# Kernel optimization log

Hardware: AMD Instinct MI355X
Metric: run time of the kernel (lower is better)

Reference implementation:

```python
import jax, jax.numpy as jnp
import numpy as np

N, F_IN, H, O = 4096, 512, 4, 256
ALPHA = 0.2  # leaky-relu negative slope
NEG = -9e15  # mask value for non-edges (matches DAEGC)


def setup_inputs() -> dict:
    key = jax.random.key(0)
    ks = jax.random.split(key, 9)
    x = jax.random.normal(ks[0], (N, F_IN), jnp.float32)
    adj = (jax.random.uniform(ks[1], (N, N)) < 0.01).astype(jnp.float32)
    adj = jnp.maximum(adj, jnp.eye(N, dtype=jnp.float32))
    M = jax.random.uniform(ks[2], (N, N), dtype=jnp.float32)  # proximity matrix
    s0 = 1.0 / np.sqrt(F_IN)
    s1 = 1.0 / np.sqrt(H * O)
    W0 = jax.random.normal(ks[3], (H, F_IN, O), jnp.float32) * s0
    a_self0 = jax.random.normal(ks[4], (H, O), jnp.float32) * 0.1
    a_neigh0 = jax.random.normal(ks[5], (H, O), jnp.float32) * 0.1
    W1 = jax.random.normal(ks[6], (H, H * O, O), jnp.float32) * s1
    a_self1 = jax.random.normal(ks[7], (H, O), jnp.float32) * 0.1
    a_neigh1 = jax.random.normal(ks[8], (H, O), jnp.float32) * 0.1
    return dict(x=x, adj=adj, M=M, W0=W0, a_self0=a_self0, a_neigh0=a_neigh0,
                W1=W1, a_self1=a_self1, a_neigh1=a_neigh1)


def gat_layer(x, adj, M, W, a_s, a_n, concat):
    # x: [N, F_in], W: [H, F_in, O]
    h = jnp.einsum('nf,hfo->hno', x, W)                      # [H, N, O]
    e = (jnp.einsum('hno,ho->hn', h, a_s)[:, :, None]
         + jnp.einsum('hno,ho->hn', h, a_n)[:, None, :])     # [H, N, N]
    e = jax.nn.leaky_relu(e * M[None], ALPHA)
    e = jnp.where(adj[None] > 0, e, NEG)
    attn = jax.nn.softmax(e, axis=-1)                        # masked neighbor softmax
    out = jnp.einsum('hnm,hmo->hno', attn, h)                # [H, N, O]
    if concat:
        return jax.nn.elu(out.transpose(1, 0, 2).reshape(x.shape[0], -1))  # [N, H*O]
    return out.mean(axis=0)                                  # [N, O]


def reference(x, adj, M, W0, a_self0, a_neigh0, W1, a_self1, a_neigh1):
    h = gat_layer(x, adj, M, W0, a_self0, a_neigh0, True)
    h = gat_layer(h, adj, M, W1, a_self1, a_neigh1, False)
    # F.normalize(h, p=2, dim=1) with eps=1e-12
    z = h / jnp.maximum(jnp.linalg.norm(h, axis=1, keepdims=True), 1e-12)
    A_pred = jax.nn.sigmoid(z @ z.T)                          # dot-product decode [N, N]
    return (A_pred, z)
```

## Files before the change

### kernel.cpp

```cpp
#include <hip/hip_runtime.h>
#include <hip/hip_bf16.h>
#include <math.h>

#define N_NODES 4096
#define F_IN0   512
#define HEADS   4
#define O_DIM   256
#define HO      1024
#define LRELU_A 0.2f
#define MAXE    192
#define LOG2E   1.44269504088896f

typedef __bf16 bf16_t;
typedef bf16_t bf16x8 __attribute__((ext_vector_type(8)));
typedef float f32x4 __attribute__((ext_vector_type(4)));
typedef unsigned short u16x8 __attribute__((ext_vector_type(8)));

__device__ __forceinline__ unsigned short f2b(float f) {
    __hip_bfloat16 t = __float2bfloat16(f);
    return __builtin_bit_cast(unsigned short, t);
}
__device__ __forceinline__ float b2f(unsigned short u) {
    unsigned int v = ((unsigned int)u) << 16;
    return __builtin_bit_cast(float, v);
}
__device__ __forceinline__ float fexp(float x) {
    return __builtin_amdgcn_exp2f(x * LOG2E);
}
__device__ __forceinline__ float fsigmoid(float x) {
    return __builtin_amdgcn_rcpf(1.f + __builtin_amdgcn_exp2f(-x * LOG2E));
}

#define GLOAD_LDS(g, l) \
    __builtin_amdgcn_global_load_lds((const __attribute__((address_space(1))) unsigned int*)(g), \
                                     (__attribute__((address_space(3))) unsigned int*)(l), 16, 0, 0)

__device__ __forceinline__ void transpose_tile(const float* __restrict__ W,
                                               unsigned short* __restrict__ Wt,
                                               int K, int O, int kt, int ot, int h,
                                               float (*t)[33], int tid) {
    const float* Wh = W + (size_t)h * K * O;
    unsigned short* Wth = Wt + (size_t)h * K * O;
    const int k0 = kt * 32, o0 = ot * 32;
    const int tx = tid & 31, ty = tid >> 5;
    for (int r = ty; r < 32; r += 8) t[r][tx] = Wh[(size_t)(k0 + r) * O + o0 + tx];
    __syncthreads();
    for (int r = ty; r < 32; r += 8)
        Wth[(size_t)(o0 + r) * K + k0 + tx] = f2b(t[tx][r]);
}

__global__ __launch_bounds__(256) void conv_k(const float* __restrict__ x,
                                              const float* __restrict__ W0,
                                              const float* __restrict__ W1,
                                              unsigned short* __restrict__ xb,
                                              unsigned short* __restrict__ wt0,
                                              unsigned short* __restrict__ wt1) {
    __shared__ float t[32][33];
    const int b = blockIdx.x;
    const int tid = threadIdx.x;
    if (b < 2048) {
        int i = b * 256 + tid;
        float4 v = ((const float4*)x)[i];
        ushort4 o;
        o.x = f2b(v.x); o.y = f2b(v.y); o.z = f2b(v.z); o.w = f2b(v.w);
        ((ushort4*)xb)[i] = o;
    } else if (b < 2560) {
        int b2 = b - 2048;
        transpose_tile(W0, wt0, F_IN0, O_DIM, (b2 & 15), ((b2 >> 4) & 7), b2 >> 7, t, tid);
    } else {
        int b2 = b - 2560;
        transpose_tile(W1, wt1, HO, O_DIM, (b2 & 31), ((b2 >> 5) & 7), b2 >> 8, t, tid);
    }
}

__global__ __launch_bounds__(256) void edge_k(const float* __restrict__ adj,
                                              int* __restrict__ ecnt,
                                              int* __restrict__ eidx) {
    const int w    = threadIdx.x >> 6;
    const int lane = threadIdx.x & 63;
    const int n    = blockIdx.x * 4 + w;
    const float* adjr = adj + (size_t)n * N_NODES;
    float4 a4[16];
#pragma unroll
    for (int it = 0; it < 16; ++it)
        a4[it] = *(const float4*)&adjr[lane * 4 + it * 256];
    unsigned long long mask = 0;
#pragma unroll
    for (int it = 0; it < 16; ++it) {
        if (a4[it].x > 0.f) mask |= 1ull << (it * 4 + 0);
        if (a4[it].y > 0.f) mask |= 1ull << (it * 4 + 1);
        if (a4[it].z > 0.f) mask |= 1ull << (it * 4 + 2);
        if (a4[it].w > 0.f) mask |= 1ull << (it * 4 + 3);
    }
    const int ec = __popcll(mask);
    int sc = ec;
#pragma unroll
    for (int off = 1; off < 64; off <<= 1) {
        int u = __shfl_up(sc, off, 64);
        if (lane >= off) sc += u;
    }
    int base = sc - ec;
    unsigned long long mm = mask;
    while (mm) {
        const int q = __builtin_ctzll(mm);
        mm &= mm - 1;
        const int m = lane * 4 + ((q >> 2) << 8) + (q & 3);
        eidx[(size_t)n * MAXE + base] = m;
        ++base;
    }
    if (lane == 63) ecnt[n] = sc;
}

__global__ __launch_bounds__(256) void mfma_nt(const bf16_t* __restrict__ A,
                                               const bf16_t* __restrict__ B,
                                               unsigned short* __restrict__ Cv,
                                               int K, int ldc,
                                               unsigned long long bStride,
                                               unsigned long long cStride) {
    B += blockIdx.z * bStride;
    const size_t zoff = (size_t)blockIdx.z * cStride;
    __shared__ bf16_t sA[128 * 32];
    __shared__ bf16_t sB[128 * 32];
    const int tid  = threadIdx.x;
    const int lane = tid & 63;
    const int wave = tid >> 6;
    const int wr = (wave >> 1) * 64;
    const int wc = (wave & 1) * 64;
    const int rowBase = blockIdx.x * 128;
    const int colBase = blockIdx.y * 128;
    const int l15  = lane & 15;
    const int quad = lane >> 4;

    const int sm = tid & 127;
    const int sc = tid >> 7;
    const bf16_t* aRow = A + (size_t)(rowBase + sm) * K + sc * 8;
    const bf16_t* bRow = B + (size_t)(colBase + sm) * K + sc * 8;
    bf16_t* sA0 = &sA[(tid & ~63) * 8];
    bf16_t* sA1 = &sA[(256 + (tid & ~63)) * 8];
    bf16_t* sB0 = &sB[(tid & ~63) * 8];
    bf16_t* sB1 = &sB[(256 + (tid & ~63)) * 8];

    f32x4 acc[4][4] = {};

    for (int k0 = 0; k0 < K; k0 += 32) {
        GLOAD_LDS(aRow + k0,      sA0);
        GLOAD_LDS(aRow + k0 + 16, sA1);
        GLOAD_LDS(bRow + k0,      sB0);
        GLOAD_LDS(bRow + k0 + 16, sB1);
        __syncthreads();
        bf16x8 af[4], bfr[4];
#pragma unroll
        for (int i = 0; i < 4; ++i) {
            af[i]  = *(bf16x8*)&sA[(quad * 128 + wr + i * 16 + l15) * 8];
            bfr[i] = *(bf16x8*)&sB[(quad * 128 + wc + i * 16 + l15) * 8];
        }
#pragma unroll
        for (int i = 0; i < 4; ++i)
#pragma unroll
            for (int j = 0; j < 4; ++j)
                acc[i][j] = __builtin_amdgcn_mfma_f32_16x16x32_bf16(af[i], bfr[j], acc[i][j], 0, 0, 0);
        __syncthreads();
    }

    const int orow = rowBase + wr + quad * 4;
    const int ocol = colBase + wc + l15;
#pragma unroll
    for (int i = 0; i < 4; ++i)
#pragma unroll
        for (int j = 0; j < 4; ++j)
#pragma unroll
            for (int r = 0; r < 4; ++r)
                Cv[zoff + (size_t)(orow + i * 16 + r) * ldc + ocol + j * 16] = f2b(acc[i][j][r]);
}

#define EP_STRIDE 132
__global__ __launch_bounds__(256) void decode_k(const bf16_t* __restrict__ Z,
                                                float* __restrict__ out) {
    __shared__ float smem_f[32 * EP_STRIDE];
    bf16_t* sA = (bf16_t*)smem_f;
    bf16_t* sB = (bf16_t*)(smem_f + 2048);
    float*  sE = smem_f;

    const int tid  = threadIdx.x;
    const int lane = tid & 63;
    const int wave = tid >> 6;
    const int wr = (wave >> 1) * 64;
    const int wc = (wave & 1) * 64;
    const int rowBase = blockIdx.x * 128;
    const int colBase = blockIdx.y * 128;
    const int l15  = lane & 15;
    const int quad = lane >> 4;

    const int sm = tid & 127;
    const int sc = tid >> 7;
    const bf16_t* aRow = Z + (size_t)(rowBase + sm) * O_DIM + sc * 8;
    const bf16_t* bRow = Z + (size_t)(colBase + sm) * O_DIM + sc * 8;
    bf16_t* sA0 = &sA[(tid & ~63) * 8];
    bf16_t* sA1 = &sA[(256 + (tid & ~63)) * 8];
    bf16_t* sB0 = &sB[(tid & ~63) * 8];
    bf16_t* sB1 = &sB[(256 + (tid & ~63)) * 8];

    f32x4 acc[4][4] = {};

    for (int k0 = 0; k0 < O_DIM; k0 += 32) {
        GLOAD_LDS(aRow + k0,      sA0);
        GLOAD_LDS(aRow + k0 + 16, sA1);
        GLOAD_LDS(bRow + k0,      sB0);
        GLOAD_LDS(bRow + k0 + 16, sB1);
        __syncthreads();
        bf16x8 af[4], bfr[4];
#pragma unroll
        for (int i = 0; i < 4; ++i) {
            af[i]  = *(bf16x8*)&sA[(quad * 128 + wr + i * 16 + l15) * 8];
            bfr[i] = *(bf16x8*)&sB[(quad * 128 + wc + i * 16 + l15) * 8];
        }
#pragma unroll
        for (int i = 0; i < 4; ++i)
#pragma unroll
            for (int j = 0; j < 4; ++j)
                acc[i][j] = __builtin_amdgcn_mfma_f32_16x16x32_bf16(af[i], bfr[j], acc[i][j], 0, 0, 0);
        __syncthreads();
    }

    const int lrBase = (wave >> 1) * 16;
    for (int i = 0; i < 4; ++i) {
#pragma unroll
        for (int j = 0; j < 4; ++j)
#pragma unroll
            for (int r = 0; r < 4; ++r)
                sE[(lrBase + quad * 4 + r) * EP_STRIDE + wc + j * 16 + l15] = acc[i][j][r];
        __syncthreads();
#pragma unroll
        for (int p = 0; p < 4; ++p) {
            const int idx4 = p * 256 + tid;
            const int lr = idx4 >> 5;
            const int c4 = idx4 & 31;
            f32x4 v = *(f32x4*)&sE[lr * EP_STRIDE + c4 * 4];
            f32x4 o;
            o[0] = fsigmoid(v[0]); o[1] = fsigmoid(v[1]);
            o[2] = fsigmoid(v[2]); o[3] = fsigmoid(v[3]);
            const int grow = rowBase + (lr >> 4) * 64 + i * 16 + (lr & 15);
            *(f32x4*)&out[(size_t)grow * N_NODES + colBase + c4 * 4] = o;
        }
        __syncthreads();
    }
}

__global__ __launch_bounds__(256) void scores_k(const unsigned short* __restrict__ hb,
                                                const float* __restrict__ a_s,
                                                const float* __restrict__ a_n,
                                                float* __restrict__ s_self4,
                                                float* __restrict__ s_neigh4) {
    const int n = blockIdx.x;
    const int head = threadIdx.x >> 6;
    const int lane = threadIdx.x & 63;
    const ushort4 hv = *(const ushort4*)&hb[(size_t)n * HO + head * O_DIM + lane * 4];
    const float4 av = *(const float4*)&a_s[head * O_DIM + lane * 4];
    const float4 nv = *(const float4*)&a_n[head * O_DIM + lane * 4];
    float h0 = b2f(hv.x), h1 = b2f(hv.y), h2 = b2f(hv.z), h3 = b2f(hv.w);
    float ps = h0 * av.x + h1 * av.y + h2 * av.z + h3 * av.w;
    float pn = h0 * nv.x + h1 * nv.y + h2 * nv.z + h3 * nv.w;
    for (int off = 32; off; off >>= 1) {
        ps += __shfl_down(ps, off, 64);
        pn += __shfl_down(pn, off, 64);
    }
    if (lane == 0) {
        s_self4[n * HEADS + head]  = ps;
        s_neigh4[n * HEADS + head] = pn;
    }
}

__global__ __launch_bounds__(256) void attn_k(const unsigned short* __restrict__ hb,
                                              const int* __restrict__ ecnt,
                                              const int* __restrict__ eidx,
                                              const float* __restrict__ Mm,
                                              const float* __restrict__ s_self4,
                                              const float* __restrict__ s_neigh4,
                                              unsigned short* __restrict__ out0,
                                              float* __restrict__ out1, int layer) {
    const int n = blockIdx.x;
    const int tid = threadIdx.x;
    __shared__ int midx[MAXE];
    __shared__ float ev[MAXE][HEADS];
    __shared__ float red2[2][HO];
    const int c = ecnt[n];

    if (tid < c) {
        const int m = eidx[(size_t)n * MAXE + tid];
        const float Mv = Mm[((size_t)n << 12) + m];
        midx[tid] = m;
        const float4 ss = *(const float4*)&s_self4[n * HEADS];
        const float4 sn = *(const float4*)&s_neigh4[m * HEADS];
        float e0 = (ss.x + sn.x) * Mv, e1 = (ss.y + sn.y) * Mv;
        float e2 = (ss.z + sn.z) * Mv, e3 = (ss.w + sn.w) * Mv;
        ev[tid][0] = e0 > 0.f ? e0 : LRELU_A * e0;
        ev[tid][1] = e1 > 0.f ? e1 : LRELU_A * e1;
        ev[tid][2] = e2 > 0.f ? e2 : LRELU_A * e2;
        ev[tid][3] = e3 > 0.f ? e3 : LRELU_A * e3;
    }
    __syncthreads();

    {
        const int w = tid >> 6, lane = tid & 63;
        float mx = -1e30f;
        for (int k = lane; k < c; k += 64) mx = fmaxf(mx, ev[k][w]);
        for (int off = 32; off; off >>= 1) mx = fmaxf(mx, __shfl_xor(mx, off, 64));
        float s = 0.f;
        for (int k = lane; k < c; k += 64) {
            float p = fexp(ev[k][w] - mx);
            ev[k][w] = p;
            s += p;
        }
        for (int off = 32; off; off >>= 1) s += __shfl_xor(s, off, 64);
        float inv = __builtin_amdgcn_rcpf(s);
        for (int k = lane; k < c; k += 64) ev[k][w] *= inv;
    }
    __syncthreads();

    const int half = tid >> 7;
    const int t    = tid & 127;
    const int hh   = t >> 5;
    float acc[8] = {};
#pragma unroll 2
    for (int k = half; k < c; k += 2) {
        const int m = midx[k];
        const float w = ev[k][hh];
        const u16x8 hv = *(const u16x8*)&hb[(size_t)m * HO + t * 8];
#pragma unroll
        for (int j = 0; j < 8; ++j) acc[j] += w * b2f(hv[j]);
    }
#pragma unroll
    for (int j = 0; j < 8; ++j) red2[half][t * 8 + j] = acc[j];
    __syncthreads();

    if (layer == 0) {
        const int o = tid * 4;
        ushort4 ov;
        float v0 = red2[0][o + 0] + red2[1][o + 0];
        float v1 = red2[0][o + 1] + red2[1][o + 1];
        float v2 = red2[0][o + 2] + red2[1][o + 2];
        float v3 = red2[0][o + 3] + red2[1][o + 3];
        ov.x = f2b(v0 > 0.f ? v0 : fexp(v0) - 1.f);
        ov.y = f2b(v1 > 0.f ? v1 : fexp(v1) - 1.f);
        ov.z = f2b(v2 > 0.f ? v2 : fexp(v2) - 1.f);
        ov.w = f2b(v3 > 0.f ? v3 : fexp(v3) - 1.f);
        *(ushort4*)&out0[(size_t)n * HO + o] = ov;
    } else {
        const int o = tid;
        float v = 0.f;
#pragma unroll
        for (int h = 0; h < HEADS; ++h)
            v += red2[0][h * O_DIM + o] + red2[1][h * O_DIM + o];
        out1[(size_t)n * O_DIM + o] = 0.25f * v;
    }
}

__global__ __launch_bounds__(256) void norm_k(float* __restrict__ z,
                                              unsigned short* __restrict__ zb) {
    const int n = blockIdx.x;
    const int tid = threadIdx.x;
    float v = z[(size_t)n * O_DIM + tid];
    float p = v * v;
    for (int off = 32; off; off >>= 1) p += __shfl_down(p, off, 64);
    __shared__ float wsum[4];
    if ((tid & 63) == 0) wsum[tid >> 6] = p;
    __syncthreads();
    float ssq = wsum[0] + wsum[1] + wsum[2] + wsum[3];
    float denom = fmaxf(sqrtf(ssq), 1e-12f);
    float zn = v / denom;
    z[(size_t)n * O_DIM + tid] = zn;
    zb[(size_t)n * O_DIM + tid] = f2b(zn);
}

extern "C" void kernel_launch(void* const* d_in, const int* in_sizes, int n_in,
                              void* d_out, int out_size, void* d_ws, size_t ws_size,
                              hipStream_t stream) {
    const float* x   = (const float*)d_in[0];
    const float* adj = (const float*)d_in[1];
    const float* Mm  = (const float*)d_in[2];
    const float* W0  = (const float*)d_in[3];
    const float* as0 = (const float*)d_in[4];
    const float* an0 = (const float*)d_in[5];
    const float* W1  = (const float*)d_in[6];
    const float* as1 = (const float*)d_in[7];
    const float* an1 = (const float*)d_in[8];
    float* out = (float*)d_out;

    unsigned short* hb    = (unsigned short*)d_ws;
    unsigned short* hin1b = hb + (size_t)N_NODES * HO;
    unsigned short* xb    = hin1b + (size_t)N_NODES * HO;
    unsigned short* wt0   = xb + (size_t)N_NODES * F_IN0;
    unsigned short* wt1   = wt0 + HEADS * O_DIM * F_IN0;
    unsigned short* zb    = wt1 + HEADS * O_DIM * HO;
    float* s_self4  = (float*)(zb + (size_t)N_NODES * O_DIM);
    float* s_neigh4 = s_self4 + N_NODES * HEADS;
    int*   eidx = (int*)(s_neigh4 + N_NODES * HEADS);
    int*   ecnt = eidx + (size_t)N_NODES * MAXE;
    float* zbuf = out + (size_t)N_NODES * N_NODES;

    conv_k<<<3584, 256, 0, stream>>>(x, W0, W1, xb, wt0, wt1);
    edge_k<<<1024, 256, 0, stream>>>(adj, ecnt, eidx);

    mfma_nt<<<dim3(32, 2, 4), 256, 0, stream>>>((const bf16_t*)xb, (const bf16_t*)wt0, hb,
                                                F_IN0, HO,
                                                (unsigned long long)O_DIM * F_IN0,
                                                (unsigned long long)O_DIM);
    scores_k<<<N_NODES, 256, 0, stream>>>(hb, as0, an0, s_self4, s_neigh4);
    attn_k<<<N_NODES, 256, 0, stream>>>(hb, ecnt, eidx, Mm, s_self4, s_neigh4, hin1b, nullptr, 0);

    mfma_nt<<<dim3(32, 2, 4), 256, 0, stream>>>((const bf16_t*)hin1b, (const bf16_t*)wt1, hb,
                                                HO, HO,
                                                (unsigned long long)O_DIM * HO,
                                                (unsigned long long)O_DIM);
    scores_k<<<N_NODES, 256, 0, stream>>>(hb, as1, an1, s_self4, s_neigh4);
    attn_k<<<N_NODES, 256, 0, stream>>>(hb, ecnt, eidx, Mm, s_self4, s_neigh4, nullptr, zbuf, 1);

    norm_k<<<N_NODES, 256, 0, stream>>>(zbuf, zb);
    decode_k<<<dim3(32, 32), 256, 0, stream>>>((const bf16_t*)zb, out);
}
```

Measured before the change: 322.8 us.

## Double-buffer LDS loads in GEMM and decode, shrink GEMM tiles to 64x64

The projection GEMM moves from 128x128 tiles to 64x64 tiles with a double-buffered LDS pipeline, quadrupling the grid to 1024 blocks for better CU occupancy. The decode GEMM also double-buffers its global-to-LDS loads so the next K slice is fetched while MFMAs run on the current one, with shared memory enlarged to hold two stages. Smaller tiles lower per-block data reuse and raise global traffic, and the larger LDS footprint in decode may reduce occupancy.

```diff
diff --git a/kernel.cpp b/kernel.cpp
--- a/kernel.cpp
+++ b/kernel.cpp
@@ -119,8 +119,67 @@
                                                unsigned long long cStride) {
     B += blockIdx.z * bStride;
     const size_t zoff = (size_t)blockIdx.z * cStride;
-    __shared__ bf16_t sA[128 * 32];
-    __shared__ bf16_t sB[128 * 32];
+    __shared__ bf16_t sAB[2][2][64 * 32];
+    const int tid  = threadIdx.x;
+    const int lane = tid & 63;
+    const int wave = tid >> 6;
+    const int wr = (wave >> 1) * 32;
+    const int wc = (wave & 1) * 32;
+    const int rowBase = blockIdx.x * 64;
+    const int colBase = blockIdx.y * 64;
+    const int l15  = lane & 15;
+    const int quad = lane >> 4;
+
+    const int sm = tid & 63;
+    const int sc = tid >> 6;
+    const bf16_t* aRow = A + (size_t)(rowBase + sm) * K + sc * 8;
+    const bf16_t* bRow = B + (size_t)(colBase + sm) * K + sc * 8;
+
+    f32x4 acc[2][2] = {};
+
+    GLOAD_LDS(aRow, &sAB[0][0][tid * 8]);
+    GLOAD_LDS(bRow, &sAB[0][1][tid * 8]);
+    __syncthreads();
+
+    int cur = 0;
+    for (int k0 = 0; k0 < K; k0 += 32) {
+        if (k0 + 32 < K) {
+            GLOAD_LDS(aRow + k0 + 32, &sAB[cur ^ 1][0][tid * 8]);
+            GLOAD_LDS(bRow + k0 + 32, &sAB[cur ^ 1][1][tid * 8]);
+        }
+        bf16x8 af[2], bfr[2];
+#pragma unroll
+        for (int i = 0; i < 2; ++i) {
+            af[i]  = *(bf16x8*)&sAB[cur][0][(quad * 64 + wr + i * 16 + l15) * 8];
+            bfr[i] = *(bf16x8*)&sAB[cur][1][(quad * 64 + wc + i * 16 + l15) * 8];
+        }
+#pragma unroll
+        for (int i = 0; i < 2; ++i)
+#pragma unroll
+            for (int j = 0; j < 2; ++j)
+                acc[i][j] = __builtin_amdgcn_mfma_f32_16x16x32_bf16(af[i], bfr[j], acc[i][j], 0, 0, 0);
+        __syncthreads();
+        cur ^= 1;
+    }
+
+    const int orow = rowBase + wr + quad * 4;
+    const int ocol = colBase + wc + l15;
+#pragma unroll
+    for (int i = 0; i < 2; ++i)
+#pragma unroll
+        for (int j = 0; j < 2; ++j)
+#pragma unroll
+            for (int r = 0; r < 4; ++r)
+                Cv[zoff + (size_t)(orow + i * 16 + r) * ldc + ocol + j * 16] = f2b(acc[i][j][r]);
+}
+
+#define EP_STRIDE 132
+__global__ __launch_bounds__(256) void decode_k(const bf16_t* __restrict__ Z,
+                                                float* __restrict__ out) {
+    __shared__ float smem_f[8192];
+    bf16_t* base = (bf16_t*)smem_f;
+    float*  sE = smem_f;
+
     const int tid  = threadIdx.x;
     const int lane = tid & 63;
     const int wave = tid >> 6;
@@ -133,21 +192,28 @@
 
     const int sm = tid & 127;
     const int sc = tid >> 7;
-    const bf16_t* aRow = A + (size_t)(rowBase + sm) * K + sc * 8;
-    const bf16_t* bRow = B + (size_t)(colBase + sm) * K + sc * 8;
-    bf16_t* sA0 = &sA[(tid & ~63) * 8];
-    bf16_t* sA1 = &sA[(256 + (tid & ~63)) * 8];
-    bf16_t* sB0 = &sB[(tid & ~63) * 8];
-    bf16_t* sB1 = &sB[(256 + (tid & ~63)) * 8];
+    const bf16_t* aRow = Z + (size_t)(rowBase + sm) * O_DIM + sc * 8;
+    const bf16_t* bRow = Z + (size_t)(colBase + sm) * O_DIM + sc * 8;
 
     f32x4 acc[4][4] = {};
 
-    for (int k0 = 0; k0 < K; k0 += 32) {
-        GLOAD_LDS(aRow + k0,      sA0);
-        GLOAD_LDS(aRow + k0 + 16, sA1);
-        GLOAD_LDS(bRow + k0,      sB0);
-        GLOAD_LDS(bRow + k0 + 16, sB1);
-        __syncthreads();
+    GLOAD_LDS(aRow,      base + tid * 8);
+    GLOAD_LDS(aRow + 16, base + (256 + tid) * 8);
+    GLOAD_LDS(bRow,      base + 4096 + tid * 8);
+    GLOAD_LDS(bRow + 16, base + 4096 + (256 + tid) * 8);
+    __syncthreads();
+
+    int cur = 0;
+    for (int k0 = 0; k0 < O_DIM; k0 += 32) {
+        if (k0 + 32 < O_DIM) {
+            bf16_t* nA = base + (cur ^ 1) * 8192;
+            GLOAD_LDS(aRow + k0 + 32, nA + tid * 8);
+            GLOAD_LDS(aRow + k0 + 48, nA + (256 + tid) * 8);
+            GLOAD_LDS(bRow + k0 + 32, nA + 4096 + tid * 8);
+            GLOAD_LDS(bRow + k0 + 48, nA + 4096 + (256 + tid) * 8);
+        }
+        bf16_t* sA = base + cur * 8192;
+        bf16_t* sB = sA + 4096;
         bf16x8 af[4], bfr[4];
 #pragma unroll
         for (int i = 0; i < 4; ++i) {
@@ -160,66 +226,7 @@
             for (int j = 0; j < 4; ++j)
                 acc[i][j] = __builtin_amdgcn_mfma_f32_16x16x32_bf16(af[i], bfr[j], acc[i][j], 0, 0, 0);
         __syncthreads();
-    }
-
-    const int orow = rowBase + wr + quad * 4;
-    const int ocol = colBase + wc + l15;
-#pragma unroll
-    for (int i = 0; i < 4; ++i)
-#pragma unroll
-        for (int j = 0; j < 4; ++j)
-#pragma unroll
-            for (int r = 0; r < 4; ++r)
-                Cv[zoff + (size_t)(orow + i * 16 + r) * ldc + ocol + j * 16] = f2b(acc[i][j][r]);
-}
-
-#define EP_STRIDE 132
-__global__ __launch_bounds__(256) void decode_k(const bf16_t* __restrict__ Z,
-                                                float* __restrict__ out) {
-    __shared__ float smem_f[32 * EP_STRIDE];
-    bf16_t* sA = (bf16_t*)smem_f;
-    bf16_t* sB = (bf16_t*)(smem_f + 2048);
-    float*  sE = smem_f;
-
-    const int tid  = threadIdx.x;
-    const int lane = tid & 63;
-    const int wave = tid >> 6;
-    const int wr = (wave >> 1) * 64;
-    const int wc = (wave & 1) * 64;
-    const int rowBase = blockIdx.x * 128;
-    const int colBase = blockIdx.y * 128;
-    const int l15  = lane & 15;
-    const int quad = lane >> 4;
-
-    const int sm = tid & 127;
-    const int sc = tid >> 7;
-    const bf16_t* aRow = Z + (size_t)(rowBase + sm) * O_DIM + sc * 8;
-    const bf16_t* bRow = Z + (size_t)(colBase + sm) * O_DIM + sc * 8;
-    bf16_t* sA0 = &sA[(tid & ~63) * 8];
-    bf16_t* sA1 = &sA[(256 + (tid & ~63)) * 8];
-    bf16_t* sB0 = &sB[(tid & ~63) * 8];
-    bf16_t* sB1 = &sB[(256 + (tid & ~63)) * 8];
-
-    f32x4 acc[4][4] = {};
-
-    for (int k0 = 0; k0 < O_DIM; k0 += 32) {
-        GLOAD_LDS(aRow + k0,      sA0);
-        GLOAD_LDS(aRow + k0 + 16, sA1);
-        GLOAD_LDS(bRow + k0,      sB0);
-        GLOAD_LDS(bRow + k0 + 16, sB1);
-        __syncthreads();
-        bf16x8 af[4], bfr[4];
-#pragma unroll
-        for (int i = 0; i < 4; ++i) {
-            af[i]  = *(bf16x8*)&sA[(quad * 128 + wr + i * 16 + l15) * 8];
-            bfr[i] = *(bf16x8*)&sB[(quad * 128 + wc + i * 16 + l15) * 8];
-        }
-#pragma unroll
-        for (int i = 0; i < 4; ++i)
-#pragma unroll
-            for (int j = 0; j < 4; ++j)
-                acc[i][j] = __builtin_amdgcn_mfma_f32_16x16x32_bf16(af[i], bfr[j], acc[i][j], 0, 0, 0);
-        __syncthreads();
+        cur ^= 1;
     }
 
     const int lrBase = (wave >> 1) * 16;
@@ -401,14 +408,14 @@
     conv_k<<<3584, 256, 0, stream>>>(x, W0, W1, xb, wt0, wt1);
     edge_k<<<1024, 256, 0, stream>>>(adj, ecnt, eidx);
 
-    mfma_nt<<<dim3(32, 2, 4), 256, 0, stream>>>((const bf16_t*)xb, (const bf16_t*)wt0, hb,
+    mfma_nt<<<dim3(64, 4, 4), 256, 0, stream>>>((const bf16_t*)xb, (const bf16_t*)wt0, hb,
                                                 F_IN0, HO,
                                                 (unsigned long long)O_DIM * F_IN0,
                                                 (unsigned long long)O_DIM);
     scores_k<<<N_NODES, 256, 0, stream>>>(hb, as0, an0, s_self4, s_neigh4);
     attn_k<<<N_NODES, 256, 0, stream>>>(hb, ecnt, eidx, Mm, s_self4, s_neigh4, hin1b, nullptr, 0);
 
-    mfma_nt<<<dim3(32, 2, 4), 256, 0, stream>>>((const bf16_t*)hin1b, (const bf16_t*)wt1, hb,
+    mfma_nt<<<dim3(64, 4, 4), 256, 0, stream>>>((const bf16_t*)hin1b, (const bf16_t*)wt1, hb,
                                                 HO, HO,
                                                 (unsigned long long)O_DIM * HO,
                                                 (unsigned long long)O_DIM);
```

After: 324.3 us. Within noise of the previous version (+0.5%).
